# Kernel tuning notes

Measured on AMD Instinct MI355X. Metric: run time of the kernel, lower is better.

The kernel has to match this reference:

```python
import jax, jax.numpy as jnp
from jax import lax
import numpy as np

NUM_SCALES = 4
NUM_ORI = 8
SIGMA = 2.0
FILTER_SIZE = 32  # min(512 // 2**scale, 32) == 32 for all scales, already even
J = 4
POOL = 2 ** J  # 16


def _make_gabor_filters():
    """Replicates GaborWavelet2D + _init_wavelet_filters. Returns (real, imag) stacks
    of shape [num_scales*num_ori, 1, FILTER_SIZE, FILTER_SIZE]."""
    oris = np.linspace(0.0, np.pi, NUM_ORI)
    idx = np.arange(FILTER_SIZE, dtype=np.float32) - FILTER_SIZE // 2
    X, Y = np.meshgrid(idx, idx, indexing='ij')
    reals, imags = [], []
    for scale in range(1, NUM_SCALES + 1):
        for o in oris:
            Xr = X * np.cos(o) + Y * np.sin(o)
            Yr = -X * np.sin(o) + Y * np.cos(o)
            sf = scale * SIGMA
            env = np.exp(-0.5 * (Xr ** 2 + Yr ** 2) / sf ** 2)
            phase = 2.0 * np.pi * (1.0 / scale) * Xr / sf
            reals.append(env * np.cos(phase))
            imags.append(env * np.sin(phase))
    real = np.stack(reals).astype(np.float32)[:, None]  # [32,1,32,32]
    imag = np.stack(imags).astype(np.float32)[:, None]
    return real, imag


def setup_inputs() -> dict:
    key = jax.random.key(0)
    x = jax.random.normal(key, (8, 3, 512, 512), dtype=jnp.float32)
    w_real, w_imag = _make_gabor_filters()
    return {"x": x, "w_real": jnp.asarray(w_real), "w_imag": jnp.asarray(w_imag)}


def _avg_pool(t):
    # torch F.avg_pool2d(kernel=16), default stride=kernel, floor mode (drop remainder)
    B, C, H, W = t.shape
    Ho, Wo = H // POOL, W // POOL
    t = t[:, :, :Ho * POOL, :Wo * POOL]
    return t.reshape(B, C, Ho, POOL, Wo, POOL).mean(axis=(3, 5))


def reference(x, w_real, w_imag):
    # x: [B,3,512,512]
    x_gray = x.mean(axis=1, keepdims=True)  # [B,1,H,W]
    S0 = _avg_pool(x_gray)  # [B,1,32,32]

    pad = FILTER_SIZE // 2  # 16 -> conv output is (H+1, W+1) = 513x513
    w = jnp.concatenate([w_real, w_imag], axis=0)  # [64,1,32,32]
    conv = lax.conv_general_dilated(
        x_gray, w, window_strides=(1, 1), padding=((pad, pad), (pad, pad)),
        dimension_numbers=('NCHW', 'OIHW', 'NCHW'))  # [B,64,513,513], cross-correlation like torch
    nf = w_real.shape[0]
    cr, ci = conv[:, :nf], conv[:, nf:]
    mag = jnp.sqrt(cr ** 2 + ci ** 2 + 1e-8)  # [B,32,513,513]
    S1 = _avg_pool(mag)  # [B,32,32,32]
    return (S0, S1)
```

## Files before the change

### kernel.cpp

```cpp
#include <hip/hip_runtime.h>
#include <math.h>

#define IMG   512
#define NFILT 32
#define NPAIR 16
#define PI_F  3.14159265358979323846f
#define GS    104

typedef _Float16 v8h __attribute__((ext_vector_type(8)));
typedef float    v4f __attribute__((ext_vector_type(4)));

__device__ __forceinline__ unsigned pkrtz(float a, float b) {
    typedef __fp16 f16x2 __attribute__((ext_vector_type(2)));
    union { f16x2 h; unsigned u; } x;
    x.h = __builtin_amdgcn_cvt_pkrtz(a, b);
    return x.u;
}

template <int CTRL>
__device__ __forceinline__ float dpp_add(float v) {
    int t = __builtin_amdgcn_update_dpp(0, __float_as_int(v), CTRL, 0xf, 0xf, true);
    return v + __int_as_float(t);
}

__device__ __forceinline__ float xor32_add(float m) {
    float a = m, b = m;
    asm("v_permlane32_swap_b32 %0, %1" : "+v"(a), "+v"(b));
    return a + b;
}

#if __has_builtin(__builtin_amdgcn_sqrtf)
__device__ __forceinline__ float fsqrt(float x) { return __builtin_amdgcn_sqrtf(x); }
#else
__device__ __forceinline__ float fsqrt(float x) { return sqrtf(x); }
#endif

__device__ __forceinline__ void bar_lgkm() {
    asm volatile("s_waitcnt lgkmcnt(0)\n\ts_barrier" ::: "memory");
}

__device__ __forceinline__ v8h ldfrag(const uint4* p) {
    union { uint4 u; v8h h; } x; x.u = *p; return x.h;
}

__global__ void make_tables(unsigned* __restrict__ tabs) {
    __shared__ _Float16 P[5][168];
    const int fo = blockIdx.x;
    const int tid = threadIdx.x;
    for (int e = tid; e < 5 * 168; e += 256) ((_Float16*)P)[e] = (_Float16)0.0f;
    __syncthreads();
    if (tid < 160) {
        int tbl = tid >> 5, t = tid & 31;
        int s = (fo >> 3) + 1, o = fo & 7;
        float theta = (float)o * (PI_F / 7.0f);
        float sf = (float)s * 2.0f;
        float kf = 2.0f * PI_F / ((float)s * sf);
        float a = kf * cosf(theta), b = kf * sinf(theta);
        float d = (float)(t - 16);
        float env = expf(-0.5f * d * d / (sf * sf));
        float v;
        switch (tbl) {
            case 0: v =  env * cosf(b * d); break;
            case 1: v =  env * sinf(b * d); break;
            case 2: v =  env * cosf(a * d); break;
            case 3: v =  env * sinf(a * d); break;
            default: v = -env * sinf(a * d); break;
        }
        P[tbl][t + 64] = (_Float16)v;
    }
    __syncthreads();
    unsigned* dst = tabs + (size_t)fo * 3200;
    for (int e = tid; e < 3200; e += 256) {
        int tbl  = e / 640;  int rem2 = e - tbl * 640;
        int copy = rem2 / 80; int idw = rem2 - copy * 80;
        int p0 = (idw >> 2) * 8 + copy + (idw & 3) * 2;
        union { unsigned u; _Float16 h[2]; } p;
        p.h[0] = P[tbl][p0];
        p.h[1] = P[tbl][p0 + 1];
        dst[e] = p.u;
    }
}

__launch_bounds__(512, 4)
__global__ void conv_kernel(const float* __restrict__ x,
                            const uint4* __restrict__ tabs,
                            float* __restrict__ s0out,
                            float* __restrict__ s1out) {
    __shared__ _Float16 gray[96 * GS];
    __shared__ _Float16 Tre[2][64 * GS];
    __shared__ _Float16 Tim[2][64 * GS];
    __shared__ float    s1st[NFILT * 16];

    const int bx = blockIdx.x;
    const int n  = bx >> 6;
    const int t6 = bx & 63;
    const int ty = t6 >> 3, tx = t6 & 7;
    const int r0g = ty * 64 - 16;
    const int c0g = tx * 64 - 16;
    const int tid = threadIdx.x;

    const int lane = tid & 63;
    const int w    = tid >> 6;
    const int r4   = w & 3;
    const int half = w >> 2;
    const int nn   = lane & 15;
    const int q8   = (lane >> 4) << 3;
    const int q4   = (lane >> 4) << 2;
    const int cr   = r4 * 16 + nn;
    const int u    = q8 - cr + 64;
    const int b0   = r4 >> 1;
    const int uoff = (u & 7) * 20 + (u >> 3);

    const uint4* fb0 = tabs + uoff;
    v8h Gre0[2], Gim0[2], Fre[2], Fim[2];
    #pragma unroll
    for (int j = 0; j < 2; ++j) {
        int idx = (b0 + j) * 4;
        Gre0[j] = ldfrag(fb0 + idx);
        Gim0[j] = ldfrag(fb0 + 160 + idx);
        Fre[j]  = ldfrag(fb0 + 320 + idx);
        Fim[j]  = ldfrag(fb0 + 480 + idx);
    }

    {
        const float* c0p = x + (size_t)n * 3 * IMG * IMG;
        const float* c1p = c0p + IMG * IMG;
        const float* c2p = c0p + 2 * IMG * IMG;
        for (int e = tid; e < 96 * 24; e += 512) {
            int hr = e / 24, g4 = e - hr * 24;
            int hc0 = g4 * 4;
            int gr = r0g + hr, gc0 = c0g + hc0;
            float4 v = make_float4(0.f, 0.f, 0.f, 0.f);
            if (hr < 95 && (unsigned)gr < IMG && (unsigned)gc0 < IMG) {
                size_t off = ((size_t)gr * IMG + gc0) >> 2;
                float4 a = ((const float4*)c0p)[off];
                float4 b = ((const float4*)c1p)[off];
                float4 c = ((const float4*)c2p)[off];
                v.x = (a.x + b.x + c.x) * (1.0f / 3.0f);
                v.y = (a.y + b.y + c.y) * (1.0f / 3.0f);
                v.z = (a.z + b.z + c.z) * (1.0f / 3.0f);
                v.w = (hc0 == 92) ? 0.0f : (a.w + b.w + c.w) * (1.0f / 3.0f);
            }
            uint2 w2;
            w2.x = pkrtz(v.x, v.y);
            w2.y = pkrtz(v.z, v.w);
            *(uint2*)(&gray[hr * GS + hc0]) = w2;
        }
    }
    __syncthreads();

    if (tid < 256) {
        int cell = tid >> 4, sub = tid & 15;
        int pr = cell >> 2, pc = cell & 3;
        const _Float16* row = &gray[(16 + pr * 16 + sub) * GS + 16 + pc * 16];
        float s = 0.0f;
        #pragma unroll
        for (int j = 0; j < 16; ++j) s += (float)row[j];
        s += __shfl_xor(s, 1);
        s += __shfl_xor(s, 2);
        s += __shfl_xor(s, 4);
        s += __shfl_xor(s, 8);
        if (sub == 0)
            s0out[(size_t)n * 1024 + (ty * 4 + pr) * 32 + (tx * 4 + pc)] = s * (1.0f / 256.0f);
    }


    v8h Agray[3][2];
    #pragma unroll
    for (int mi = 0; mi < 3; ++mi)
        #pragma unroll
        for (int j = 0; j < 2; ++j)
            Agray[mi][j] = *(const v8h*)(&gray[((half * 3 + mi) * 16 + nn) * GS + (b0 + j) * 32 + q8]);

    #pragma unroll
    for (int mi = 0; mi < 3; ++mi) {
        int mt = half * 3 + mi;
        v4f aR = {0.f, 0.f, 0.f, 0.f}, aI = {0.f, 0.f, 0.f, 0.f};
        #pragma unroll
        for (int j = 0; j < 2; ++j) {
            aR = __builtin_amdgcn_mfma_f32_16x16x32_f16(Agray[mi][j], Gre0[j], aR, 0, 0, 0);
            aI = __builtin_amdgcn_mfma_f32_16x16x32_f16(Agray[mi][j], Gim0[j], aI, 0, 0, 0);
        }
        int mb = mt * 16 + q4;
        uint2 pr, pi;
        pr.x = pkrtz(aR[0], aR[1]);  pr.y = pkrtz(aR[2], aR[3]);
        pi.x = pkrtz(aI[0], aI[1]);  pi.y = pkrtz(aI[2], aI[3]);
        *(uint2*)(&Tre[0][cr * GS + mb]) = pr;
        *(uint2*)(&Tim[0][cr * GS + mb]) = pi;
    }
    __syncthreads();

    for (int p = 0; p < NPAIR; ++p) {
        const _Float16* Tr  = Tre[p & 1];
        const _Float16* Ti  = Tim[p & 1];
        _Float16*       Trn = Tre[(p + 1) & 1];
        _Float16*       Tin = Tim[(p + 1) & 1];
        const int fa  = ((p >> 2) << 3) + (p & 3);
        const int fbi = ((p >> 2) << 3) + 7 - (p & 3);
        const int nxp = (p < NPAIR - 1) ? p + 1 : p;
        const int nxfa = ((nxp >> 2) << 3) + (nxp & 3);
        const uint4* fbn = tabs + (size_t)nxfa * 800 + uoff;

        v8h Gre[2], Gim[2];
        #pragma unroll
        for (int j = 0; j < 2; ++j) {
            int idx = (b0 + j) * 4;
            Gre[j] = ldfrag(fbn + idx);
            Gim[j] = ldfrag(fbn + 160 + idx);
        }

        #pragma unroll
        for (int ni = 0; ni < 2; ++ni) {
            int nt = half * 2 + ni;
            v4f P1 = {0.f, 0.f, 0.f, 0.f}, P2 = {0.f, 0.f, 0.f, 0.f};
            v4f P3 = {0.f, 0.f, 0.f, 0.f}, P4 = {0.f, 0.f, 0.f, 0.f};
            #pragma unroll
            for (int j = 0; j < 2; ++j) {
                v8h tR = *(const v8h*)(&Tr[(nt * 16 + nn) * GS + (b0 + j) * 32 + q8]);
                v8h tI = *(const v8h*)(&Ti[(nt * 16 + nn) * GS + (b0 + j) * 32 + q8]);
                P1 = __builtin_amdgcn_mfma_f32_16x16x32_f16(Fre[j], tR, P1, 0, 0, 0);
                P2 = __builtin_amdgcn_mfma_f32_16x16x32_f16(Fim[j], tI, P2, 0, 0, 0);
                P3 = __builtin_amdgcn_mfma_f32_16x16x32_f16(Fre[j], tI, P3, 0, 0, 0);
                P4 = __builtin_amdgcn_mfma_f32_16x16x32_f16(Fim[j], tR, P4, 0, 0, 0);
            }
            v4f are = P1 - P2, aim = P3 + P4;
            v4f bre = P1 + P2, bim = P3 - P4;
            float sa0 = fsqrt(fmaf(are[0], are[0], fmaf(aim[0], aim[0], 1e-8f)));
            float sa1 = fsqrt(fmaf(are[1], are[1], fmaf(aim[1], aim[1], 1e-8f)));
            float sa2 = fsqrt(fmaf(are[2], are[2], fmaf(aim[2], aim[2], 1e-8f)));
            float sa3 = fsqrt(fmaf(are[3], are[3], fmaf(aim[3], aim[3], 1e-8f)));
            float sb0 = fsqrt(fmaf(bre[0], bre[0], fmaf(bim[0], bim[0], 1e-8f)));
            float sb1 = fsqrt(fmaf(bre[1], bre[1], fmaf(bim[1], bim[1], 1e-8f)));
            float sb2 = fsqrt(fmaf(bre[2], bre[2], fmaf(bim[2], bim[2], 1e-8f)));
            float sb3 = fsqrt(fmaf(bre[3], bre[3], fmaf(bim[3], bim[3], 1e-8f)));
            float ma = (sa0 + sa1) + (sa2 + sa3);
            float mb = (sb0 + sb1) + (sb2 + sb3);
            ma = dpp_add<0xB1>(ma);   mb = dpp_add<0xB1>(mb);
            ma = dpp_add<0x4E>(ma);   mb = dpp_add<0x4E>(mb);
            ma = dpp_add<0x141>(ma);  mb = dpp_add<0x141>(mb);
            ma = dpp_add<0x140>(ma);  mb = dpp_add<0x140>(mb);
            ma += __shfl_xor(ma, 16); mb += __shfl_xor(mb, 16);
            ma = xor32_add(ma);       mb = xor32_add(mb);
            if (lane == 0) {
                s1st[fa  * 16 + r4 * 4 + nt] = ma;
                s1st[fbi * 16 + r4 * 4 + nt] = mb;
            }
        }

        if (p < NPAIR - 1) {
            #pragma unroll
            for (int mi = 0; mi < 3; ++mi) {
                int mt = half * 3 + mi;
                v4f aR = {0.f, 0.f, 0.f, 0.f}, aI = {0.f, 0.f, 0.f, 0.f};
                #pragma unroll
                for (int j = 0; j < 2; ++j) {
                    aR = __builtin_amdgcn_mfma_f32_16x16x32_f16(Agray[mi][j], Gre[j], aR, 0, 0, 0);
                    aI = __builtin_amdgcn_mfma_f32_16x16x32_f16(Agray[mi][j], Gim[j], aI, 0, 0, 0);
                }
                int mb = mt * 16 + q4;
                uint2 pr, pi;
                pr.x = pkrtz(aR[0], aR[1]);  pr.y = pkrtz(aR[2], aR[3]);
                pi.x = pkrtz(aI[0], aI[1]);  pi.y = pkrtz(aI[2], aI[3]);
                *(uint2*)(&Trn[cr * GS + mb]) = pr;
                *(uint2*)(&Tin[cr * GS + mb]) = pi;
            }
            #pragma unroll
            for (int j = 0; j < 2; ++j) {
                int idx = (b0 + j) * 4;
                Fre[j] = ldfrag(fbn + 320 + idx);
                Fim[j] = ldfrag(fbn + 480 + idx);
            }
        }
        bar_lgkm();
    }

    float* s1b = s1out + (size_t)n * NFILT * 32 * 32;
    for (int e = tid; e < NFILT * 16; e += 512) {
        int fi = e >> 4, cell = e & 15;
        int r4c = cell >> 2, ntc = cell & 3;
        s1b[((size_t)fi * 32 + (ty * 4 + r4c)) * 32 + (tx * 4 + ntc)] =
            s1st[e] * (1.0f / 256.0f);
    }
}

extern "C" void kernel_launch(void* const* d_in, const int* in_sizes, int n_in,
                              void* d_out, int out_size, void* d_ws, size_t ws_size,
                              hipStream_t stream) {
    const float* x = (const float*)d_in[0];
    float* out = (float*)d_out;
    unsigned* tabs = (unsigned*)d_ws;

    hipLaunchKernelGGL(make_tables, dim3(32), dim3(256), 0, stream, tabs);
    hipLaunchKernelGGL(conv_kernel, dim3(512), dim3(512), 0, stream,
                       x, (const uint4*)tabs, out, out + 8192);
}
```

Baseline: 113.3 us.

## Swizzle LDS intermediate layout and restructure magnitude computation

Applies an XOR swizzle to the column index of the shared-memory Tre/Tim intermediate on both the write and read paths, to cut LDS bank conflicts. Replaces the paired sum/difference magnitude computation with vector squared-norm arithmetic (|a|^2 = s ± 2t), clamped to 1e-8 before sqrt. Replaces the permlane32 swap with a shfl_xor by 32. The algebraic form can lose precision through cancellation, and the swizzle only works if reads and writes agree on the mapping.

Measured after the change: 118.3 us. +4.4%, slower.

```diff
diff --git a/kernel.cpp b/kernel.cpp
--- a/kernel.cpp
+++ b/kernel.cpp
@@ -21,12 +21,6 @@
 __device__ __forceinline__ float dpp_add(float v) {
     int t = __builtin_amdgcn_update_dpp(0, __float_as_int(v), CTRL, 0xf, 0xf, true);
     return v + __int_as_float(t);
-}
-
-__device__ __forceinline__ float xor32_add(float m) {
-    float a = m, b = m;
-    asm("v_permlane32_swap_b32 %0, %1" : "+v"(a), "+v"(b));
-    return a + b;
 }
 
 #if __has_builtin(__builtin_amdgcn_sqrtf)
@@ -110,6 +104,8 @@
     const int u    = q8 - cr + 64;
     const int b0   = r4 >> 1;
     const int uoff = (u & 7) * 20 + (u >> 3);
+    const int hx8  = (((lane >> 4) ^ (nn & 3)) << 3);
+    const int crx3 = cr & 3;
 
     const uint4* fb0 = tabs + uoff;
     v8h Gre0[2], Gim0[2], Fre[2], Fim[2];
@@ -164,7 +160,6 @@
             s0out[(size_t)n * 1024 + (ty * 4 + pr) * 32 + (tx * 4 + pc)] = s * (1.0f / 256.0f);
     }
 
-
     v8h Agray[3][2];
     #pragma unroll
     for (int mi = 0; mi < 3; ++mi)
@@ -181,12 +176,13 @@
             aR = __builtin_amdgcn_mfma_f32_16x16x32_f16(Agray[mi][j], Gre0[j], aR, 0, 0, 0);
             aI = __builtin_amdgcn_mfma_f32_16x16x32_f16(Agray[mi][j], Gim0[j], aI, 0, 0, 0);
         }
-        int mb = mt * 16 + q4;
+        int gw = (((mt << 1) | (q4 >> 3)) ^ crx3);
+        int wo = cr * GS + gw * 8 + (q4 & 7);
         uint2 pr, pi;
         pr.x = pkrtz(aR[0], aR[1]);  pr.y = pkrtz(aR[2], aR[3]);
         pi.x = pkrtz(aI[0], aI[1]);  pi.y = pkrtz(aI[2], aI[3]);
-        *(uint2*)(&Tre[0][cr * GS + mb]) = pr;
-        *(uint2*)(&Tim[0][cr * GS + mb]) = pi;
+        *(uint2*)(&Tre[0][wo]) = pr;
+        *(uint2*)(&Tim[0][wo]) = pi;
     }
     __syncthreads();
 
@@ -216,23 +212,30 @@
             v4f P3 = {0.f, 0.f, 0.f, 0.f}, P4 = {0.f, 0.f, 0.f, 0.f};
             #pragma unroll
             for (int j = 0; j < 2; ++j) {
-                v8h tR = *(const v8h*)(&Tr[(nt * 16 + nn) * GS + (b0 + j) * 32 + q8]);
-                v8h tI = *(const v8h*)(&Ti[(nt * 16 + nn) * GS + (b0 + j) * 32 + q8]);
+                int ro = (nt * 16 + nn) * GS + (b0 + j) * 32 + hx8;
+                v8h tR = *(const v8h*)(&Tr[ro]);
+                v8h tI = *(const v8h*)(&Ti[ro]);
                 P1 = __builtin_amdgcn_mfma_f32_16x16x32_f16(Fre[j], tR, P1, 0, 0, 0);
                 P2 = __builtin_amdgcn_mfma_f32_16x16x32_f16(Fim[j], tI, P2, 0, 0, 0);
                 P3 = __builtin_amdgcn_mfma_f32_16x16x32_f16(Fre[j], tI, P3, 0, 0, 0);
                 P4 = __builtin_amdgcn_mfma_f32_16x16x32_f16(Fim[j], tR, P4, 0, 0, 0);
             }
-            v4f are = P1 - P2, aim = P3 + P4;
-            v4f bre = P1 + P2, bim = P3 - P4;
-            float sa0 = fsqrt(fmaf(are[0], are[0], fmaf(aim[0], aim[0], 1e-8f)));
-            float sa1 = fsqrt(fmaf(are[1], are[1], fmaf(aim[1], aim[1], 1e-8f)));
-            float sa2 = fsqrt(fmaf(are[2], are[2], fmaf(aim[2], aim[2], 1e-8f)));
-            float sa3 = fsqrt(fmaf(are[3], are[3], fmaf(aim[3], aim[3], 1e-8f)));
-            float sb0 = fsqrt(fmaf(bre[0], bre[0], fmaf(bim[0], bim[0], 1e-8f)));
-            float sb1 = fsqrt(fmaf(bre[1], bre[1], fmaf(bim[1], bim[1], 1e-8f)));
-            float sb2 = fsqrt(fmaf(bre[2], bre[2], fmaf(bim[2], bim[2], 1e-8f)));
-            float sb3 = fsqrt(fmaf(bre[3], bre[3], fmaf(bim[3], bim[3], 1e-8f)));
+            const v4f eps4 = {1e-8f, 1e-8f, 1e-8f, 1e-8f};
+            v4f s4 = P1 * P1 + eps4;
+            s4 = P2 * P2 + s4;
+            s4 = P3 * P3 + s4;
+            s4 = P4 * P4 + s4;
+            v4f t4 = P1 * P2 - P3 * P4;
+            t4 = t4 + t4;
+            v4f na = s4 - t4, nb = s4 + t4;
+            float sa0 = fsqrt(fmaxf(na[0], 1e-8f));
+            float sa1 = fsqrt(fmaxf(na[1], 1e-8f));
+            float sa2 = fsqrt(fmaxf(na[2], 1e-8f));
+            float sa3 = fsqrt(fmaxf(na[3], 1e-8f));
+            float sb0 = fsqrt(fmaxf(nb[0], 1e-8f));
+            float sb1 = fsqrt(fmaxf(nb[1], 1e-8f));
+            float sb2 = fsqrt(fmaxf(nb[2], 1e-8f));
+            float sb3 = fsqrt(fmaxf(nb[3], 1e-8f));
             float ma = (sa0 + sa1) + (sa2 + sa3);
             float mb = (sb0 + sb1) + (sb2 + sb3);
             ma = dpp_add<0xB1>(ma);   mb = dpp_add<0xB1>(mb);
@@ -240,7 +243,7 @@
             ma = dpp_add<0x141>(ma);  mb = dpp_add<0x141>(mb);
             ma = dpp_add<0x140>(ma);  mb = dpp_add<0x140>(mb);
             ma += __shfl_xor(ma, 16); mb += __shfl_xor(mb, 16);
-            ma = xor32_add(ma);       mb = xor32_add(mb);
+            ma += __shfl_xor(ma, 32); mb += __shfl_xor(mb, 32);
             if (lane == 0) {
                 s1st[fa  * 16 + r4 * 4 + nt] = ma;
                 s1st[fbi * 16 + r4 * 4 + nt] = mb;
@@ -257,12 +260,13 @@
                     aR = __builtin_amdgcn_mfma_f32_16x16x32_f16(Agray[mi][j], Gre[j], aR, 0, 0, 0);
                     aI = __builtin_amdgcn_mfma_f32_16x16x32_f16(Agray[mi][j], Gim[j], aI, 0, 0, 0);
                 }
-                int mb = mt * 16 + q4;
+                int gw = (((mt << 1) | (q4 >> 3)) ^ crx3);
+                int wo = cr * GS + gw * 8 + (q4 & 7);
                 uint2 pr, pi;
                 pr.x = pkrtz(aR[0], aR[1]);  pr.y = pkrtz(aR[2], aR[3]);
                 pi.x = pkrtz(aI[0], aI[1]);  pi.y = pkrtz(aI[2], aI[3]);
-                *(uint2*)(&Trn[cr * GS + mb]) = pr;
-                *(uint2*)(&Tin[cr * GS + mb]) = pi;
+                *(uint2*)(&Trn[wo]) = pr;
+                *(uint2*)(&Tin[wo]) = pi;
             }
             #pragma unroll
             for (int j = 0; j < 2; ++j) {
```
